# Kernel tuning notes

Hardware: AMD Instinct MI355X
Metric: run time of the kernel (lower is better)

The kernel has to match this reference:

```python
import jax, jax.numpy as jnp
import numpy as np

B, S, D = 4, 2048, 768      # batch, seq_len, embedding_dim
I = 1536                    # inner_dim = embedding_dim * up_proj_factor
H, HD = 8, 64               # num_heads, head_dim
EPS = 1e-5


def setup_inputs() -> dict:
    key = jax.random.key(0)
    ks = jax.random.split(key, 12)
    std = 0.02
    f32 = jnp.float32
    p = {}
    p["x"] = jax.random.normal(ks[0], (B, S, D), f32)
    # block LayerNorm
    p["ln_g"] = jnp.ones((D,), f32)
    p["ln_b"] = jnp.zeros((D,), f32)
    # up / down projections (bias-free, as in the module)
    p["W_up"] = jax.random.normal(ks[1], (D, I), f32) * std
    p["W_down"] = jax.random.normal(ks[2], (I, D), f32) * std
    # mLSTM cell: q/k/v projections to num_heads*head_dim
    p["Wq"] = jax.random.normal(ks[3], (I, H * HD), f32) * std
    p["Wk"] = jax.random.normal(ks[4], (I, H * HD), f32) * std
    p["Wv"] = jax.random.normal(ks[5], (I, H * HD), f32) * std
    # scalar per-head input / forget gate pre-activations
    p["Wi"] = jax.random.normal(ks[6], (I, H), f32) * std
    p["bi"] = jnp.zeros((H,), f32)
    p["Wf"] = jax.random.normal(ks[7], (I, H), f32) * std
    p["bf"] = 3.0 * jnp.ones((H,), f32)  # positive forget-gate bias init
    # output gate and cell output projection
    p["Wo"] = jax.random.normal(ks[8], (I, H * HD), f32) * std
    p["bo"] = jnp.zeros((H * HD,), f32)
    p["mh_g"] = jnp.ones((H, HD), f32)  # per-head norm scale (group norm)
    p["W_out"] = jax.random.normal(ks[9], (H * HD, I), f32) * std
    return p


def _forward(x, ln_g, ln_b, W_up, Wq, Wk, Wv, Wi, bi, Wf, bf, Wo, bo, mh_g, W_out, W_down):
    resid = x
    # LayerNorm
    mu = x.mean(-1, keepdims=True)
    var = ((x - mu) ** 2).mean(-1, keepdims=True)
    h = (x - mu) * jax.lax.rsqrt(var + EPS) * ln_g + ln_b
    # up projection
    u = h @ W_up                                    # (B,S,I)
    # mLSTM projections
    q = (u @ Wq).reshape(B, S, H, HD)
    k = (u @ Wk).reshape(B, S, H, HD) * (HD ** -0.5)
    v = (u @ Wv).reshape(B, S, H, HD)
    i_raw = u @ Wi + bi                             # (B,S,H)
    f_raw = u @ Wf + bf                             # (B,S,H)

    def step(carry, inp):
        C, n, m = carry                             # C:(B,H,HD,HD) n:(B,H,HD) m:(B,H)
        qt, kt, vt, it, ft = inp
        # log-space stabilization of exponential gates
        m_new = jnp.maximum(ft + m, it)
        ig = jnp.exp(it - m_new)
        fg = jnp.exp(ft + m - m_new)
        C = fg[..., None, None] * C + ig[..., None, None] * (vt[..., :, None] * kt[..., None, :])
        n = fg[..., None] * n + ig[..., None] * kt
        num = jnp.einsum('bhvk,bhk->bhv', C, qt)
        den = jnp.maximum(jnp.abs(jnp.einsum('bhk,bhk->bh', n, qt)), 1.0)
        return (C, n, m_new), num / den[..., None]

    xs = (jnp.moveaxis(q, 1, 0), jnp.moveaxis(k, 1, 0), jnp.moveaxis(v, 1, 0),
          jnp.moveaxis(i_raw, 1, 0), jnp.moveaxis(f_raw, 1, 0))
    C0 = jnp.zeros((B, H, HD, HD), x.dtype)
    n0 = jnp.zeros((B, H, HD), x.dtype)
    m0 = jnp.zeros((B, H), x.dtype)
    _, hts = jax.lax.scan(step, (C0, n0, m0), xs)   # (S,B,H,HD)
    ht = jnp.moveaxis(hts, 0, 1)                    # (B,S,H,HD)
    # per-head normalization (group norm, scale only)
    mu2 = ht.mean(-1, keepdims=True)
    var2 = ((ht - mu2) ** 2).mean(-1, keepdims=True)
    hn = (ht - mu2) * jax.lax.rsqrt(var2 + EPS) * mh_g
    # output gate + cell output projection
    o = jax.nn.sigmoid(u @ Wo + bo).reshape(B, S, H, HD)
    y = (o * hn).reshape(B, S, H * HD) @ W_out      # (B,S,I)
    # down projection + residual (dropout=0 -> identity)
    return resid + y @ W_down


def reference(x, ln_g, ln_b, W_up, Wq, Wk, Wv, Wi, bi, Wf, bf, Wo, bo, mh_g, W_out, W_down):
    return _forward(x, ln_g, ln_b, W_up, Wq, Wk, Wv, Wi, bi, Wf, bf, Wo, bo, mh_g, W_out, W_down)
```

## Files before the change

### kernel.cpp

```cpp
#include <hip/hip_runtime.h>
#include <hip/hip_bf16.h>
#include <stdint.h>
#include <stddef.h>

typedef __bf16 bf16_t;
typedef __bf16 bf16x4 __attribute__((ext_vector_type(4)));
typedef __bf16 bf16x8 __attribute__((ext_vector_type(8)));
typedef float  f32x4  __attribute__((ext_vector_type(4)));

#define Bsz  4
#define Ssz  2048
#define Dsz  768
#define Isz  1536
#define Hn   8
#define HDsz 64
#define NTOK (Bsz*Ssz)
#define Lc   64
#define NCH  (Ssz/Lc)
#define NBH  (Bsz*Hn)
#define NUX  1664

#define OFF_H      ((size_t)0)
#define OFF_WUPX   ((size_t)12582912)
#define OFF_WQX    ((size_t)15138816)
#define OFF_WDOWNT ((size_t)21430272)
#define OFF_WOC    ((size_t)23789568)
#define OFF_BIAS   ((size_t)24576000)
#define OFF_U      ((size_t)24580096)
#define OFF_QKVO   ((size_t)49745920)
#define OFF_KT     ((size_t)83300352)
#define OFF_VT     ((size_t)91688960)
#define OFF_IFB    ((size_t)100077568)
#define OFF_BLOC   ((size_t)100601856)
#define OFF_MHAT   ((size_t)100864000)
#define OFF_MST    ((size_t)101126144)
#define OFF_DEC    ((size_t)101130240)
#define OFF_MEND   ((size_t)101134336)
#define OFF_NG     ((size_t)101138432)
#define OFF_NST    ((size_t)101400576)
#define OFF_WOCP   ((size_t)0)
#define OFF_CSTB   ((size_t)0)
#define OFF_WOUTB  OFF_QKVO
#define OFF_G      OFF_U
#define OFF_GATED  (OFF_U + 16777216)

__device__ __forceinline__ void gload16(const void* gsrc, void* ldst) {
  __builtin_amdgcn_global_load_lds(
      (const __attribute__((address_space(1))) void*)gsrc,
      (__attribute__((address_space(3))) void*)ldst, 16, 0, 0);
}

__device__ __forceinline__ float blockReduceSum256(float v) {
  #pragma unroll
  for (int o = 1; o < 64; o <<= 1) v += __shfl_xor(v, o, 64);
  __shared__ float sh[4];
  int wid = threadIdx.x >> 6;
  __syncthreads();
  if ((threadIdx.x & 63) == 0) sh[wid] = v;
  __syncthreads();
  return sh[0] + sh[1] + sh[2] + sh[3];
}

__global__ __launch_bounds__(256) void prep_weights(
    const float* __restrict__ W_up, const float* __restrict__ Wq,
    const float* __restrict__ Wk, const float* __restrict__ Wv,
    const float* __restrict__ Wo, const float* __restrict__ W_down,
    const float* __restrict__ W_out, const float* __restrict__ bo,
    const float* __restrict__ bi, const float* __restrict__ bfv,
    bf16_t* __restrict__ wupxT, bf16_t* __restrict__ wqxT,
    bf16_t* __restrict__ wdownT, bf16_t* __restrict__ woutB,
    float* __restrict__ biasA) {
  __shared__ float tile[32][33];
  const int bid = blockIdx.x;
  const int tx = threadIdx.x, ty = threadIdx.y;
  const float* src; bf16_t* dst; int K, N, bx, by; float scale = 1.f;
  if (bid < 1152)      { int l = bid;        src = W_up;   dst = wupxT;                       K = 768;  N = 1536; bx = l % 48; by = l / 48; }
  else if (bid < 1920) { int l = bid - 1152; src = Wq;     dst = wqxT;                        K = 1536; N = 512;  bx = l % 16; by = l / 16; }
  else if (bid < 2688) { int l = bid - 1920; src = Wk;     dst = wqxT + (size_t)512 * Isz;    K = 1536; N = 512;  bx = l % 16; by = l / 16; scale = 0.125f; }
  else if (bid < 3456) { int l = bid - 2688; src = Wv;     dst = wqxT + (size_t)1024 * Isz;   K = 1536; N = 512;  bx = l % 16; by = l / 16; }
  else if (bid < 4224) { int l = bid - 3456; src = Wo;     dst = wqxT + (size_t)1536 * Isz;   K = 1536; N = 512;  bx = l % 16; by = l / 16; }
  else if (bid < 5376) { int l = bid - 4224; src = W_down; dst = wdownT;                      K = 1536; N = 768;  bx = l % 24; by = l / 24; }
  else if (bid < 6144) {
    int base = (bid - 5376) * 1024 + (ty * 32 + tx) * 4;
    #pragma unroll
    for (int e = 0; e < 4; ++e) woutB[base + e] = (bf16_t)W_out[base + e];
    return;
  } else {
    int tid = ty * 32 + tx;
    for (int i = tid; i < 528; i += 256)
      biasA[i] = (i < 512) ? bo[i] : ((i < 520) ? bi[i - 512] : bfv[i - 520]);
    return;
  }
  int n0 = bx * 32, k0 = by * 32;
  #pragma unroll
  for (int j = 0; j < 32; j += 8)
    tile[ty + j][tx] = src[(size_t)(k0 + ty + j) * N + n0 + tx];
  __syncthreads();
  #pragma unroll
  for (int j = 0; j < 32; j += 8)
    dst[(size_t)(n0 + ty + j) * K + k0 + tx] = (bf16_t)(tile[tx][ty + j] * scale);
}

__global__ __launch_bounds__(64) void build_wuif(const float* __restrict__ W_up,
                                                 const float* __restrict__ Wi,
                                                 const float* __restrict__ Wf,
                                                 bf16_t* __restrict__ dst ) {
  int d = blockIdx.x;
  int lane = threadIdx.x;
  float acc[16];
  #pragma unroll
  for (int j = 0; j < 16; ++j) acc[j] = 0.f;
  for (int i = lane; i < Isz; i += 64) {
    float w = W_up[(size_t)d * Isz + i];
    f32x4 wi0 = *(const f32x4*)&Wi[(size_t)i * 8];
    f32x4 wi1 = *(const f32x4*)&Wi[(size_t)i * 8 + 4];
    f32x4 wf0 = *(const f32x4*)&Wf[(size_t)i * 8];
    f32x4 wf1 = *(const f32x4*)&Wf[(size_t)i * 8 + 4];
    #pragma unroll
    for (int j = 0; j < 4; ++j) {
      acc[j]      += w * wi0[j];
      acc[4 + j]  += w * wi1[j];
      acc[8 + j]  += w * wf0[j];
      acc[12 + j] += w * wf1[j];
    }
  }
  #pragma unroll
  for (int j = 0; j < 16; ++j)
    #pragma unroll
    for (int o = 1; o < 64; o <<= 1) acc[j] += __shfl_xor(acc[j], o, 64);
  if (lane == 0) {
    #pragma unroll
    for (int j = 0; j < 16; ++j)
      dst[(size_t)j * Dsz + d] = (bf16_t)acc[j];
  }
}

__global__ __launch_bounds__(256) void ln_kernel(const float* __restrict__ x,
                                                 const float* __restrict__ g,
                                                 const float* __restrict__ bta,
                                                 bf16_t* __restrict__ h) {
  size_t tok = blockIdx.x;
  const float* xr = x + tok * Dsz;
  int t = threadIdx.x;
  float v[3]; float s = 0.f;
  #pragma unroll
  for (int i = 0; i < 3; ++i) { v[i] = xr[t + 256 * i]; s += v[i]; }
  s = blockReduceSum256(s);
  float mu = s * (1.f / Dsz);
  float s2 = 0.f;
  #pragma unroll
  for (int i = 0; i < 3; ++i) { float d = v[i] - mu; s2 += d * d; }
  s2 = blockReduceSum256(s2);
  float rs = rsqrtf(s2 * (1.f / Dsz) + 1e-5f);
  #pragma unroll
  for (int i = 0; i < 3; ++i) {
    int col = t + 256 * i;
    h[tok * Dsz + col] = (bf16_t)((v[i] - mu) * rs * g[col] + bta[col]);
  }
}

template<int EPI>
__global__ __launch_bounds__(512, 4) void gemm_mn(const bf16_t* __restrict__ A,
                                                  const bf16_t* __restrict__ Bt,
                                                  void* __restrict__ Cout,
                                                  const void* __restrict__ extra,
                                                  bf16_t* __restrict__ kTg,
                                                  bf16_t* __restrict__ vTg,
                                                  float* __restrict__ ifb,
                                                  int M, int N, int K) {
  __shared__ bf16_t As[256 * 64];
  __shared__ bf16_t Bs[128 * 64];
  const int t = threadIdx.x;
  const int w = t >> 6, l = t & 63;
  const int wm = w >> 1, wn = w & 1;
  const int l15 = l & 15, l4 = l >> 4;

  const int gx = gridDim.x;
  const int nwg = gx * gridDim.y;
  const int cpx = nwg >> 3;
  int bid = blockIdx.y * gx + blockIdx.x;
  int wg = (bid & 7) * cpx + (bid >> 3);
  const int tile_m = (wg / gx) * 256;
  const int tile_n = (wg % gx) * 128;

  f32x4 acc[4][4];
  #pragma unroll
  for (int m = 0; m < 4; ++m)
    #pragma unroll
    for (int n = 0; n < 4; ++n) acc[m][n] = (f32x4){0.f, 0.f, 0.f, 0.f};

  for (int k0 = 0; k0 < K; k0 += 64) {
    #pragma unroll
    for (int j = 0; j < 4; ++j) {
      int c = t + j * 512;
      int row = c >> 3;
      int ec = ((c & 7) * 8) ^ ((row & 7) << 3);
      gload16(A + (size_t)(tile_m + row) * K + k0 + ec, (char*)As + (size_t)c * 16);
    }
    #pragma unroll
    for (int j = 0; j < 2; ++j) {
      int c = t + j * 512;
      int row = c >> 3;
      int ec = ((c & 7) * 8) ^ ((row & 7) << 3);
      gload16(Bt + (size_t)(tile_n + row) * K + k0 + ec, (char*)Bs + (size_t)c * 16);
    }
    __syncthreads();
    #pragma unroll
    for (int kk = 0; kk < 2; ++kk) {
      bf16x8 aF[4], bF[4];
      #pragma unroll
      for (int m = 0; m < 4; ++m) {
        int r = wm * 64 + m * 16 + l15;
        aF[m] = *(const bf16x8*)((const char*)As + r * 128 + ((kk * 64 + l4 * 16) ^ ((r & 7) << 4)));
      }
      #pragma unroll
      for (int n = 0; n < 4; ++n) {
        int r = wn * 64 + n * 16 + l15;
        bF[n] = *(const bf16x8*)((const char*)Bs + r * 128 + ((kk * 64 + l4 * 16) ^ ((r & 7) << 4)));
      }
      #pragma unroll
      for (int m = 0; m < 4; ++m)
        #pragma unroll
        for (int n = 0; n < 4; ++n)
          acc[m][n] = __builtin_amdgcn_mfma_f32_16x16x32_bf16(aF[m], bF[n], acc[m][n], 0, 0, 0);
    }
    __syncthreads();
  }

  const int rbase = tile_m + wm * 64 + l4 * 4;
  const int cbase = tile_n + wn * 64 + l15;
  if constexpr (EPI == 5) {
    const float* bias = (const float*)extra;
    #pragma unroll
    for (int m = 0; m < 4; ++m) {
      int row0 = rbase + m * 16;
      int bb = row0 >> 11, s0 = row0 & 2047;
      #pragma unroll
      for (int n = 0; n < 4; ++n) {
        int col = cbase + n * 16;
        if (col < 512) {
          #pragma unroll
          for (int j = 0; j < 4; ++j)
            ((bf16_t*)Cout)[(size_t)(row0 + j) * 2048 + col] = (bf16_t)acc[m][n][j];
        } else if (col < 1024) {
          int hd = col - 512;
          bf16x4 pk;
          #pragma unroll
          for (int j = 0; j < 4; ++j) {
            bf16_t bv = (bf16_t)acc[m][n][j];
            ((bf16_t*)Cout)[(size_t)(row0 + j) * 2048 + col] = bv;
            pk[j] = bv;
          }
          *(bf16x4*)(kTg + ((size_t)(bb * 8 + (hd >> 6)) * 64 + (hd & 63)) * Ssz + s0) = pk;
        } else if (col < 1536) {
          int hd = col - 1024;
          bf16x4 pv;
          #pragma unroll
          for (int j = 0; j < 4; ++j) pv[j] = (bf16_t)acc[m][n][j];
          *(bf16x4*)(vTg + ((size_t)(bb * 8 + (hd >> 6)) * 64 + (hd & 63)) * Ssz + s0) = pv;
        } else {
          float b = bias[col - 1536];
          #pragma unroll
          for (int j = 0; j < 4; ++j) {
            float z = acc[m][n][j] + b;
            ((bf16_t*)Cout)[(size_t)(row0 + j) * 2048 + col] = (bf16_t)(1.f / (1.f + __expf(-z)));
          }
        }
      }
    }
  } else if constexpr (EPI == 6) {
    const float* bias = (const float*)extra;
    #pragma unroll
    for (int m = 0; m < 4; ++m)
      #pragma unroll
      for (int n = 0; n < 4; ++n) {
        int col = cbase + n * 16;
        if (col < 1536) {
          #pragma unroll
          for (int j = 0; j < 4; ++j)
            ((bf16_t*)Cout)[(size_t)(rbase + m * 16 + j) * 1536 + col] = (bf16_t)acc[m][n][j];
        } else if (col < 1552) {
          float b = bias[col - 1536];
          #pragma unroll
          for (int j = 0; j < 4; ++j)
            ifb[(size_t)(rbase + m * 16 + j) * 16 + (col - 1536)] = acc[m][n][j] + b;
        }
      }
  } else {
    #pragma unroll
    for (int m = 0; m < 4; ++m)
      #pragma unroll
      for (int n = 0; n < 4; ++n)
        #pragma unroll
        for (int j = 0; j < 4; ++j) {
          int row = rbase + m * 16 + j;
          int col = cbase + n * 16;
          float v = acc[m][n][j];
          if constexpr (EPI == 0) {
            ((bf16_t*)Cout)[(size_t)row * N + col] = (bf16_t)v;
          } else {
            ((float*)Cout)[(size_t)row * N + col] =
                v + ((const float*)extra)[(size_t)row * N + col];
          }
        }
  }
}

__global__ __launch_bounds__(256) void gemm_woc_part(const bf16_t* __restrict__ A,
                                                     const bf16_t* __restrict__ Bt,
                                                     float* __restrict__ P) {
  __shared__ bf16_t As[128 * 64];
  __shared__ bf16_t Bs[128 * 64];
  const int t = threadIdx.x;
  const int w = t >> 6, l = t & 63;
  const int tile_m = blockIdx.y * 128, tile_n = blockIdx.x * 128;
  const int kz = blockIdx.z;
  const int wr = w >> 1, wc = w & 1;
  const int lrow = l >> 3;
  const int lks = ((l & 7) * 8) ^ (lrow << 3);
  const int l15 = l & 15, l4 = l >> 4;

  f32x4 acc[4][4];
  #pragma unroll
  for (int m = 0; m < 4; ++m)
    #pragma unroll
    for (int n = 0; n < 4; ++n) acc[m][n] = (f32x4){0.f, 0.f, 0.f, 0.f};

  for (int k0 = kz * 192; k0 < kz * 192 + 192; k0 += 64) {
    #pragma unroll
    for (int i = 0; i < 4; ++i) {
      int ch = w * 4 + i;
      int row = ch * 8 + lrow;
      gload16(A  + (size_t)(tile_m + row) * Isz + k0 + lks, &As[ch * 512]);
      gload16(Bt + (size_t)(tile_n + row) * Isz + k0 + lks, &Bs[ch * 512]);
    }
    __syncthreads();
    #pragma unroll
    for (int kk = 0; kk < 2; ++kk) {
      bf16x8 af[4], bfr[4];
      #pragma unroll
      for (int m = 0; m < 4; ++m) {
        int r = wr * 64 + m * 16 + l15;
        af[m] = *(const bf16x8*)&As[r * 64 + ((kk * 32 + l4 * 8) ^ ((r & 7) << 3))];
      }
      #pragma unroll
      for (int n = 0; n < 4; ++n) {
        int r = wc * 64 + n * 16 + l15;
        bfr[n] = *(const bf16x8*)&Bs[r * 64 + ((kk * 32 + l4 * 8) ^ ((r & 7) << 3))];
      }
      #pragma unroll
      for (int m = 0; m < 4; ++m)
        #pragma unroll
        for (int n = 0; n < 4; ++n)
          acc[m][n] = __builtin_amdgcn_mfma_f32_16x16x32_bf16(af[m], bfr[n], acc[m][n], 0, 0, 0);
    }
    __syncthreads();
  }

  const int rbase = tile_m + wr * 64 + l4 * 4;
  const int cbase = tile_n + wc * 64 + l15;
  float* Pz = P + (size_t)kz * 768 * 512;
  #pragma unroll
  for (int m = 0; m < 4; ++m)
    #pragma unroll
    for (int n = 0; n < 4; ++n)
      #pragma unroll
      for (int j = 0; j < 4; ++j)
        Pz[(size_t)(rbase + m * 16 + j) * 512 + cbase + n * 16] = acc[m][n][j];
}

__global__ __launch_bounds__(256) void woc_reduce(const float* __restrict__ P,
                                                  bf16_t* __restrict__ wocT) {
  int i = blockIdx.x * 256 + threadIdx.x;
  float s = 0.f;
  #pragma unroll
  for (int z = 0; z < 8; ++z) s += P[(size_t)z * 393216 + i];
  wocT[i] = (bf16_t)s;
}

__global__ __launch_bounds__(64) void gates_a(const float* __restrict__ ifb,
                                              float* __restrict__ blocal,
                                              float* __restrict__ Mhat) {
  int bh = blockIdx.x >> 5, c = blockIdx.x & 31;
  int b = bh >> 3, h = bh & 7;
  int lane = threadIdx.x;
  size_t tok = (size_t)b * Ssz + c * Lc + lane;
  float iv = ifb[tok * 16 + h];
  float fv = ifb[tok * 16 + 8 + h];
  float bt = fv;
  #pragma unroll
  for (int d = 1; d < 64; d <<= 1) { float o = __shfl_up(bt, d, 64); if (lane >= d) bt += o; }
  float a = iv - bt;
  float pm = a;
  #pragma unroll
  for (int d = 1; d < 64; d <<= 1) { float o = __shfl_up(pm, d, 64); if (lane >= d) pm = fmaxf(pm, o); }
  blocal[(size_t)bh * Ssz + c * Lc + lane] = bt;
  Mhat[(size_t)bh * Ssz + c * Lc + lane] = bt + pm;
}

__global__ void gates_b(const float* __restrict__ blocal, const float* __restrict__ Mhat,
                        float* __restrict__ mstart, float* __restrict__ decays,
                        float* __restrict__ mend) {
  int bh = threadIdx.x;
  if (bh < NBH) {
    float M = 0.f;
    for (int c = 0; c < NCH; ++c) {
      mstart[bh * NCH + c] = M;
      float bL = blocal[(size_t)bh * Ssz + c * Lc + 63];
      float Mh = Mhat[(size_t)bh * Ssz + c * Lc + 63];
      float Mn = fmaxf(M + bL, Mh);
      decays[bh * NCH + c] = __expf(M + bL - Mn);
      mend[bh * NCH + c] = Mn;
      M = Mn;
    }
  }
}

__global__ __launch_bounds__(256) void chunk_inc_mfma(const bf16_t* __restrict__ kTg,
                                                      const bf16_t* __restrict__ vTg,
                                                      const float* __restrict__ ifb,
                                                      const float* __restrict__ blocal,
                                                      const float* __restrict__ mend,
                                                      bf16_t* __restrict__ G,
                                                      float* __restrict__ ng) {
  int bh = blockIdx.x >> 5, c = blockIdx.x & 31;
  int b = bh >> 3, h = bh & 7;
  __shared__ bf16_t Vt[64 * 64];
  __shared__ bf16_t Kw[64 * 64];
  __shared__ float wsh[64];
  const int t = threadIdx.x, w = t >> 6, l = t & 63;
  const int l15 = l & 15, l4 = l >> 4;
  if (t < 64) {
    float mL = mend[bh * NCH + c];
    float bL = blocal[(size_t)bh * Ssz + c * Lc + 63];
    float bt = blocal[(size_t)bh * Ssz + c * Lc + t];
    float iv = ifb[((size_t)b * Ssz + c * Lc + t) * 16 + h];
    wsh[t] = __expf(iv + bL - bt - mL);
  }
  __syncthreads();
  {
    const int r = l >> 3, c8 = (l & 7) * 8;
    #pragma unroll
    for (int i = 0; i < 2; ++i) {
      int seg = w * 2 + i, row = seg * 8 + r;
      gload16(vTg + ((size_t)bh * 64 + row) * Ssz + c * 64 + c8, &Vt[seg * 512]);
    }
    #pragma unroll
    for (int i = 0; i < 2; ++i) {
      int e = t + i * 256; int row = e >> 3, c0 = (e & 7) * 8;
      bf16x8 kv = *(const bf16x8*)(kTg + ((size_t)bh * 64 + row) * Ssz + c * 64 + c0);
      #pragma unroll
      for (int j = 0; j < 8; ++j) kv[j] = (bf16_t)((float)kv[j] * wsh[c0 + j]);
      *(bf16x8*)&Kw[row * 64 + c0] = kv;
    }
  }
  __syncthreads();
  f32x4 acc[4];
  #pragma unroll
  for (int n = 0; n < 4; ++n) acc[n] = (f32x4){0.f, 0.f, 0.f, 0.f};
  #pragma unroll
  for (int kk = 0; kk < 2; ++kk) {
    bf16x8 af = *(const bf16x8*)&Vt[(w * 16 + l15) * 64 + kk * 32 + l4 * 8];
    #pragma unroll
    for (int n = 0; n < 4; ++n) {
      bf16x8 bfr = *(const bf16x8*)&Kw[(n * 16 + l15) * 64 + kk * 32 + l4 * 8];
      acc[n] = __builtin_amdgcn_mfma_f32_16x16x32_bf16(af, bfr, acc[n], 0, 0, 0);
    }
  }
  size_t gb = ((size_t)bh * NCH + c) * 4096;
  #pragma unroll
  for (int n = 0; n < 4; ++n)
    #pragma unroll
    for (int j = 0; j < 4; ++j) {
      int row = w * 16 + l4 * 4 + j;
      int col = n * 16 + l15;
      G[gb + (size_t)row * 64 + col] = (bf16_t)acc[n][j];
    }
  if (t < 64) {
    float s = 0.f;
    for (int s2 = 0; s2 < 64; ++s2) s += (float)Kw[t * 64 + s2];
    ng[((size_t)bh * NCH + c) * 64 + t] = s;
  }
}

__global__ __launch_bounds__(256) void state_scan(const bf16_t* __restrict__ G,
                                                  const float* __restrict__ ng,
                                                  const float* __restrict__ decays,
                                                  bf16_t* __restrict__ CstB,
                                                  float* __restrict__ nst) {
  int gid = blockIdx.x;
  if (gid < 512) {
    int idx = gid * 256 + threadIdx.x;
    int bh = idx >> 12, e = idx & 4095;
    const float* d = decays + bh * NCH;
    float C = 0.f;
    #pragma unroll
    for (int c = 0; c < NCH; ++c) {
      size_t o = ((size_t)bh * NCH + c) * 4096 + e;
      CstB[o] = (bf16_t)C;
      C = d[c] * C + (float)G[o];
    }
  } else {
    int idx = (gid - 512) * 256 + threadIdx.x;
    int bh = idx >> 6, e = idx & 63;
    const float* d = decays + bh * NCH;
    float n = 0.f;
    #pragma unroll
    for (int c = 0; c < NCH; ++c) {
      size_t o = ((size_t)bh * NCH + c) * 64 + e;
      nst[o] = n;
      n = d[c] * n + ng[o];
    }
  }
}

__global__ __launch_bounds__(256) void intra_mfma(const bf16_t* __restrict__ qkvo,
                                                  const bf16_t* __restrict__ vTg,
                                                  const bf16_t* __restrict__ CstB,
                                                  const float* __restrict__ nst,
                                                  const float* __restrict__ ifb,
                                                  const float* __restrict__ blocal,
                                                  const float* __restrict__ Mhat,
                                                  const float* __restrict__ mstart,
                                                  const float* __restrict__ mhg,
                                                  bf16_t* __restrict__ gated) {
  int bh = blockIdx.x >> 5, c = blockIdx.x & 31;
  int b = bh >> 3, h = bh & 7;
  __shared__ bf16_t qs[64 * 64];
  __shared__ bf16_t ks[64 * 64];
  __shared__ bf16_t vTs[64 * 64];
  __shared__ bf16_t Cs[64 * 64];
  __shared__ float nin[64], den_s[64], ssrc[64], sdst[64], esc[64];
  const int t = threadIdx.x, w = t >> 6, l = t & 63;
  const int l15 = l & 15, l4 = l >> 4;
  const size_t tok0 = (size_t)b * Ssz + c * Lc;
  const size_t cbase = ((size_t)bh * NCH + c) * 4096;

  if (t < 64) {
    nin[t] = nst[((size_t)bh * NCH + c) * 64 + t];
    float bt = blocal[(size_t)bh * Ssz + c * Lc + t];
    float Mh2 = Mhat[(size_t)bh * Ssz + c * Lc + t];
    float Mc = mstart[bh * NCH + c];
    float iv = ifb[(tok0 + t) * 16 + h];
    float mt = fmaxf(Mc + bt, Mh2);
    ssrc[t] = iv - bt;
    sdst[t] = bt - mt;
    esc[t]  = __expf(Mc + bt - mt);
  }
  {
    const int r = l >> 3, c8 = (l & 7) * 8;
    #pragma unroll
    for (int i = 0; i < 2; ++i) {
      int seg = w * 2 + i, row = seg * 8 + r;
      gload16(qkvo + (tok0 + row) * 2048 + h * 64 + c8,          &qs[seg * 512]);
      gload16(qkvo + (tok0 + row) * 2048 + 512 + h * 64 + c8,    &ks[seg * 512]);
      gload16(vTg + ((size_t)bh * 64 + row) * Ssz + c * 64 + c8, &vTs[seg * 512]);
      gload16(CstB + cbase + seg * 512 + l * 8,                  &Cs[seg * 512]);
    }
  }
  __syncthreads();

  f32x4 aS[4];
  #pragma unroll
  for (int n = 0; n < 4; ++n) aS[n] = (f32x4){0.f, 0.f, 0.f, 0.f};
  #pragma unroll
  for (int kk = 0; kk < 2; ++kk) {
    bf16x8 af = *(const bf16x8*)&qs[(w * 16 + l15) * 64 + kk * 32 + l4 * 8];
    #pragma unroll
    for (int n = 0; n < 4; ++n) {
      bf16x8 bfr = *(const bf16x8*)&ks[(n * 16 + l15) * 64 + kk * 32 + l4 * 8];
      aS[n] = __builtin_amdgcn_mfma_f32_16x16x32_bf16(af, bfr, aS[n], 0, 0, 0);
    }
  }
  {
    int row = w * 16 + (l >> 2);
    int c0 = (l & 3) * 16;
    float e = esc[row];
    #pragma unroll
    for (int i2 = 0; i2 < 2; ++i2) {
      bf16x8 v8 = *(const bf16x8*)&qs[row * 64 + c0 + i2 * 8];
      #pragma unroll
      for (int j = 0; j < 8; ++j) v8[j] = (bf16_t)((float)v8[j] * e);
      *(bf16x8*)&qs[row * 64 + c0 + i2 * 8] = v8;
    }
  }
  float rs[4] = {0.f, 0.f, 0.f, 0.f};
  #pragma unroll
  for (int n = 0; n < 4; ++n) {
    int col = n * 16 + l15;
    float es = ssrc[col];
    #pragma unroll
    for (int j = 0; j < 4; ++j) {
      int row = w * 16 + l4 * 4 + j;
      float p = (col <= row) ? aS[n][j] * __expf(es + sdst[row]) : 0.f;
      aS[n][j] = p;
      rs[j] += p;
    }
  }
  #pragma unroll
  for (int j = 0; j < 4; ++j) {
    rs[j] += __shfl_xor(rs[j], 1, 64);
    rs[j] += __shfl_xor(rs[j], 2, 64);
    rs[j] += __shfl_xor(rs[j], 4, 64);
    rs[j] += __shfl_xor(rs[j], 8, 64);
  }
  if (l15 == 0) {
    #pragma unroll
    for (int j = 0; j < 4; ++j) den_s[w * 16 + l4 * 4 + j] = rs[j];
  }
  __syncthreads();

  #pragma unroll
  for (int n = 0; n < 4; ++n)
    #pragma unroll
    for (int j = 0; j < 4; ++j)
      ks[(w * 16 + l4 * 4 + j) * 64 + n * 16 + l15] = (bf16_t)aS[n][j];

  {
    int row = w * 16 + (l >> 2);
    int c0 = (l & 3) * 16;
    float part = 0.f;
    #pragma unroll
    for (int i2 = 0; i2 < 16; ++i2)
      part += (float)qs[row * 64 + c0 + i2] * nin[c0 + i2];
    part += __shfl_xor(part, 1, 64);
    part += __shfl_xor(part, 2, 64);
    if ((l & 3) == 0)
      den_s[row] = fmaxf(fabsf(den_s[row] + part), 1.0f);
  }
  __syncthreads();

  f32x4 aO[4];
  #pragma unroll
  for (int n = 0; n < 4; ++n) aO[n] = (f32x4){0.f, 0.f, 0.f, 0.f};
  #pragma unroll
  for (int kk = 0; kk < 2; ++kk) {
    bf16x8 afP = *(const bf16x8*)&ks[(w * 16 + l15) * 64 + kk * 32 + l4 * 8];
    bf16x8 afQ = *(const bf16x8*)&qs[(w * 16 + l15) * 64 + kk * 32 + l4 * 8];
    #pragma unroll
    for (int n = 0; n < 4; ++n) {
      bf16x8 bV = *(const bf16x8*)&vTs[(n * 16 + l15) * 64 + kk * 32 + l4 * 8];
      bf16x8 bC = *(const bf16x8*)&Cs[(n * 16 + l15) * 64 + kk * 32 + l4 * 8];
      aO[n] = __builtin_amdgcn_mfma_f32_16x16x32_bf16(afP, bV, aO[n], 0, 0, 0);
      aO[n] = __builtin_amdgcn_mfma_f32_16x16x32_bf16(afQ, bC, aO[n], 0, 0, 0);
    }
  }

  #pragma unroll
  for (int j = 0; j < 4; ++j) {
    int row = w * 16 + l4 * 4 + j;
    float rinv = 1.f / den_s[row];
    float ov[4];
    #pragma unroll
    for (int n = 0; n < 4; ++n) ov[n] = aO[n][j] * rinv;
    float s = ov[0] + ov[1] + ov[2] + ov[3];
    s += __shfl_xor(s, 1, 64); s += __shfl_xor(s, 2, 64);
    s += __shfl_xor(s, 4, 64); s += __shfl_xor(s, 8, 64);
    float mu = s * (1.f / 64.f);
    float s2 = 0.f;
    #pragma unroll
    for (int n = 0; n < 4; ++n) { float d = ov[n] - mu; s2 += d * d; }
    s2 += __shfl_xor(s2, 1, 64); s2 += __shfl_xor(s2, 2, 64);
    s2 += __shfl_xor(s2, 4, 64); s2 += __shfl_xor(s2, 8, 64);
    float rstd = rsqrtf(s2 * (1.f / 64.f) + 1e-5f);
    size_t tok = tok0 + row;
    #pragma unroll
    for (int n = 0; n < 4; ++n) {
      int colh = n * 16 + l15;
      float og = (float)qkvo[tok * 2048 + 1536 + h * 64 + colh];
      float hn = (ov[n] - mu) * rstd * mhg[h * 64 + colh];
      gated[tok * 512 + h * 64 + colh] = (bf16_t)(og * hn);
    }
  }
}

extern "C" void kernel_launch(void* const* d_in, const int* in_sizes, int n_in,
                              void* d_out, int out_size, void* d_ws, size_t ws_size,
                              hipStream_t stream) {
  const float* x     = (const float*)d_in[0];
  const float* ln_g  = (const float*)d_in[1];
  const float* ln_b  = (const float*)d_in[2];
  const float* W_up  = (const float*)d_in[3];
  const float* W_down= (const float*)d_in[4];
  const float* Wq    = (const float*)d_in[5];
  const float* Wk    = (const float*)d_in[6];
  const float* Wv    = (const float*)d_in[7];
  const float* Wi    = (const float*)d_in[8];
  const float* bi    = (const float*)d_in[9];
  const float* Wf    = (const float*)d_in[10];
  const float* bfv   = (const float*)d_in[11];
  const float* Wo    = (const float*)d_in[12];
  const float* bo    = (const float*)d_in[13];
  const float* mh_g  = (const float*)d_in[14];
  const float* W_out = (const float*)d_in[15];

  char* ws = (char*)d_ws;
  bf16_t* hbuf   = (bf16_t*)(ws + OFF_H);
  bf16_t* wupxT  = (bf16_t*)(ws + OFF_WUPX);
  bf16_t* wqxT   = (bf16_t*)(ws + OFF_WQX);
  bf16_t* wdownT = (bf16_t*)(ws + OFF_WDOWNT);
  bf16_t* wocT   = (bf16_t*)(ws + OFF_WOC);
  float*  biasA  = (float*)(ws + OFF_BIAS);
  bf16_t* ubuf   = (bf16_t*)(ws + OFF_U);
  bf16_t* qkvob  = (bf16_t*)(ws + OFF_QKVO);
  bf16_t* woutB  = (bf16_t*)(ws + OFF_WOUTB);
  float*  wocP   = (float*)(ws + OFF_WOCP);
  bf16_t* kTg    = (bf16_t*)(ws + OFF_KT);
  bf16_t* vTg    = (bf16_t*)(ws + OFF_VT);
  float*  ifb    = (float*)(ws + OFF_IFB);
  float*  bloc   = (float*)(ws + OFF_BLOC);
  float*  Mh     = (float*)(ws + OFF_MHAT);
  float*  mst    = (float*)(ws + OFF_MST);
  float*  decays = (float*)(ws + OFF_DEC);
  float*  mendb  = (float*)(ws + OFF_MEND);
  float*  ngbuf  = (float*)(ws + OFF_NG);
  float*  nst    = (float*)(ws + OFF_NST);
  bf16_t* CstB   = (bf16_t*)(ws + OFF_CSTB);
  bf16_t* Gbuf   = (bf16_t*)(ws + OFF_G);
  bf16_t* gbuf   = (bf16_t*)(ws + OFF_GATED);

  prep_weights<<<6145, dim3(32, 8), 0, stream>>>(W_up, Wq, Wk, Wv, Wo, W_down, W_out,
                                                 bo, bi, bfv, wupxT, wqxT, wdownT, woutB, biasA);
  build_wuif<<<Dsz, 64, 0, stream>>>(W_up, Wi, Wf, wupxT + (size_t)1536 * Dsz);
  gemm_woc_part<<<dim3(4, 6, 8), 256, 0, stream>>>(wdownT, woutB, wocP);
  woc_reduce<<<1536, 256, 0, stream>>>(wocP, wocT);

  ln_kernel<<<NTOK, 256, 0, stream>>>(x, ln_g, ln_b, hbuf);

  gemm_mn<6><<<dim3(NUX / 128, NTOK / 256), 512, 0, stream>>>(hbuf, wupxT, ubuf, biasA + 512, nullptr, nullptr, ifb, NTOK, NUX, Dsz);
  gemm_mn<5><<<dim3(2048 / 128, NTOK / 256), 512, 0, stream>>>(ubuf, wqxT, qkvob, biasA, kTg, vTg, nullptr, NTOK, 2048, Isz);

  gates_a<<<NBH * NCH, 64, 0, stream>>>(ifb, bloc, Mh);
  gates_b<<<1, 32, 0, stream>>>(bloc, Mh, mst, decays, mendb);
  chunk_inc_mfma<<<NBH * NCH, 256, 0, stream>>>(kTg, vTg, ifb, bloc, mendb, Gbuf, ngbuf);
  state_scan<<<520, 256, 0, stream>>>(Gbuf, ngbuf, decays, CstB, nst);
  intra_mfma<<<NBH * NCH, 256, 0, stream>>>(qkvob, vTg, CstB, nst, ifb, bloc, Mh, mst, mh_g, gbuf);

  gemm_mn<3><<<dim3(Dsz / 128, NTOK / 256), 512, 0, stream>>>(gbuf, wocT, (float*)d_out, x, nullptr, nullptr, nullptr, NTOK, Dsz, 512);
}
```

Before: 175.1 us.

## Fold W_up into q/k/v/o weights and compute gates with a small MFMA kernel

Precomputes the product of the q/k/v/o weight stack with W_up (via a split-K weight GEMM plus reduction), so the activation path goes straight from the LayerNorm output to q/k/v/o with K=768. This removes the separate up-projection GEMM and the materialised u buffer. The input and forget gate pre-activations move into a dedicated thin MFMA kernel over h. The cost is extra per-call weight-prep GEMM work and different bf16 rounding, since the product is rounded once instead of u being rounded.

```diff
diff --git a/kernel.cpp b/kernel.cpp
--- a/kernel.cpp
+++ b/kernel.cpp
@@ -18,31 +18,32 @@
 #define Lc   64
 #define NCH  (Ssz/Lc)
 #define NBH  (Bsz*Hn)
-#define NUX  1664
 
 #define OFF_H      ((size_t)0)
-#define OFF_WUPX   ((size_t)12582912)
-#define OFF_WQX    ((size_t)15138816)
-#define OFF_WDOWNT ((size_t)21430272)
-#define OFF_WOC    ((size_t)23789568)
-#define OFF_BIAS   ((size_t)24576000)
-#define OFF_U      ((size_t)24580096)
-#define OFF_QKVO   ((size_t)49745920)
-#define OFF_KT     ((size_t)83300352)
-#define OFF_VT     ((size_t)91688960)
-#define OFF_IFB    ((size_t)100077568)
-#define OFF_BLOC   ((size_t)100601856)
-#define OFF_MHAT   ((size_t)100864000)
-#define OFF_MST    ((size_t)101126144)
-#define OFF_DEC    ((size_t)101130240)
-#define OFF_MEND   ((size_t)101134336)
-#define OFF_NG     ((size_t)101138432)
-#define OFF_NST    ((size_t)101400576)
-#define OFF_WOCP   ((size_t)0)
-#define OFF_CSTB   ((size_t)0)
-#define OFF_WOUTB  OFF_QKVO
-#define OFF_G      OFF_U
-#define OFF_GATED  (OFF_U + 16777216)
+#define OFF_WQX    ((size_t)12582912)
+#define OFF_WQC    ((size_t)18874368)
+#define OFF_WDOWNT ((size_t)22020096)
+#define OFF_WOC    ((size_t)24379392)
+#define OFF_WUPB   ((size_t)25165824)
+#define OFF_WUIF   ((size_t)27525120)
+#define OFF_BIAS   ((size_t)27549696)
+#define OFF_WOUTB  ((size_t)27553792)
+#define OFF_QKVO   ((size_t)29126656)
+#define OFF_KT     ((size_t)62681088)
+#define OFF_VT     ((size_t)71069696)
+#define OFF_GATED  ((size_t)79458304)
+#define OFF_G      ((size_t)87846912)
+#define OFF_IFB    ((size_t)96235520)
+#define OFF_BLOC   ((size_t)96759808)
+#define OFF_MHAT   ((size_t)97021952)
+#define OFF_MST    ((size_t)97284096)
+#define OFF_DEC    ((size_t)97288192)
+#define OFF_MEND   ((size_t)97292288)
+#define OFF_NG     ((size_t)97296384)
+#define OFF_NST    ((size_t)97558528)
+#define OFF_WOCP   OFF_H
+#define OFF_CSTB   OFF_H
+#define OFF_COMPP  OFF_QKVO
 
 __device__ __forceinline__ void gload16(const void* gsrc, void* ldst) {
   __builtin_amdgcn_global_load_lds(
@@ -67,23 +68,27 @@
     const float* __restrict__ Wo, const float* __restrict__ W_down,
     const float* __restrict__ W_out, const float* __restrict__ bo,
     const float* __restrict__ bi, const float* __restrict__ bfv,
-    bf16_t* __restrict__ wupxT, bf16_t* __restrict__ wqxT,
-    bf16_t* __restrict__ wdownT, bf16_t* __restrict__ woutB,
+    bf16_t* __restrict__ wqxT, bf16_t* __restrict__ wdownT,
+    bf16_t* __restrict__ woutB, bf16_t* __restrict__ wupB,
     float* __restrict__ biasA) {
   __shared__ float tile[32][33];
   const int bid = blockIdx.x;
   const int tx = threadIdx.x, ty = threadIdx.y;
   const float* src; bf16_t* dst; int K, N, bx, by; float scale = 1.f;
-  if (bid < 1152)      { int l = bid;        src = W_up;   dst = wupxT;                       K = 768;  N = 1536; bx = l % 48; by = l / 48; }
-  else if (bid < 1920) { int l = bid - 1152; src = Wq;     dst = wqxT;                        K = 1536; N = 512;  bx = l % 16; by = l / 16; }
-  else if (bid < 2688) { int l = bid - 1920; src = Wk;     dst = wqxT + (size_t)512 * Isz;    K = 1536; N = 512;  bx = l % 16; by = l / 16; scale = 0.125f; }
-  else if (bid < 3456) { int l = bid - 2688; src = Wv;     dst = wqxT + (size_t)1024 * Isz;   K = 1536; N = 512;  bx = l % 16; by = l / 16; }
-  else if (bid < 4224) { int l = bid - 3456; src = Wo;     dst = wqxT + (size_t)1536 * Isz;   K = 1536; N = 512;  bx = l % 16; by = l / 16; }
-  else if (bid < 5376) { int l = bid - 4224; src = W_down; dst = wdownT;                      K = 1536; N = 768;  bx = l % 24; by = l / 24; }
-  else if (bid < 6144) {
-    int base = (bid - 5376) * 1024 + (ty * 32 + tx) * 4;
+  if (bid < 768)       { int l = bid;        src = Wq;     dst = wqxT;                      K = 1536; N = 512; bx = l % 16; by = l / 16; }
+  else if (bid < 1536) { int l = bid - 768;  src = Wk;     dst = wqxT + (size_t)512 * Isz;  K = 1536; N = 512; bx = l % 16; by = l / 16; scale = 0.125f; }
+  else if (bid < 2304) { int l = bid - 1536; src = Wv;     dst = wqxT + (size_t)1024 * Isz; K = 1536; N = 512; bx = l % 16; by = l / 16; }
+  else if (bid < 3072) { int l = bid - 2304; src = Wo;     dst = wqxT + (size_t)1536 * Isz; K = 1536; N = 512; bx = l % 16; by = l / 16; }
+  else if (bid < 4224) { int l = bid - 3072; src = W_down; dst = wdownT;                    K = 1536; N = 768; bx = l % 24; by = l / 24; }
+  else if (bid < 4992) {
+    int base = (bid - 4224) * 1024 + (ty * 32 + tx) * 4;
     #pragma unroll
     for (int e = 0; e < 4; ++e) woutB[base + e] = (bf16_t)W_out[base + e];
+    return;
+  } else if (bid < 6144) {
+    int base = (bid - 4992) * 1024 + (ty * 32 + tx) * 4;
+    #pragma unroll
+    for (int e = 0; e < 4; ++e) wupB[base + e] = (bf16_t)W_up[base + e];
     return;
   } else {
     int tid = ty * 32 + tx;
@@ -132,6 +137,81 @@
     #pragma unroll
     for (int j = 0; j < 16; ++j)
       dst[(size_t)j * Dsz + d] = (bf16_t)acc[j];
+  }
+}
+
+__global__ __launch_bounds__(256) void gemm_partk(const bf16_t* __restrict__ A,
+                                                  const bf16_t* __restrict__ Bt,
+                                                  float* __restrict__ P,
+                                                  int M, int N, int Ktot, int kslice) {
+  __shared__ bf16_t As[128 * 64];
+  __shared__ bf16_t Bs[128 * 64];
+  const int t = threadIdx.x;
+  const int w = t >> 6, l = t & 63;
+  const int tile_m = blockIdx.y * 128, tile_n = blockIdx.x * 128;
+  const int kz = blockIdx.z;
+  const int wr = w >> 1, wc = w & 1;
+  const int lrow = l >> 3;
+  const int lks = ((l & 7) * 8) ^ (lrow << 3);
+  const int l15 = l & 15, l4 = l >> 4;
+
+  f32x4 acc[4][4];
+  #pragma unroll
+  for (int m = 0; m < 4; ++m)
+    #pragma unroll
+    for (int n = 0; n < 4; ++n) acc[m][n] = (f32x4){0.f, 0.f, 0.f, 0.f};
+
+  for (int k0 = kz * kslice; k0 < kz * kslice + kslice; k0 += 64) {
+    #pragma unroll
+    for (int i = 0; i < 4; ++i) {
+      int ch = w * 4 + i;
+      int row = ch * 8 + lrow;
+      gload16(A  + (size_t)(tile_m + row) * Ktot + k0 + lks, &As[ch * 512]);
+      gload16(Bt + (size_t)(tile_n + row) * Ktot + k0 + lks, &Bs[ch * 512]);
+    }
+    __syncthreads();
+    #pragma unroll
+    for (int kk = 0; kk < 2; ++kk) {
+      bf16x8 af[4], bfr[4];
+      #pragma unroll
+      for (int m = 0; m < 4; ++m) {
+        int r = wr * 64 + m * 16 + l15;
+        af[m] = *(const bf16x8*)&As[r * 64 + ((kk * 32 + l4 * 8) ^ ((r & 7) << 3))];
+      }
+      #pragma unroll
+      for (int n = 0; n < 4; ++n) {
+        int r = wc * 64 + n * 16 + l15;
+        bfr[n] = *(const bf16x8*)&Bs[r * 64 + ((kk * 32 + l4 * 8) ^ ((r & 7) << 3))];
+      }
+      #pragma unroll
+      for (int m = 0; m < 4; ++m)
+        #pragma unroll
+        for (int n = 0; n < 4; ++n)
+          acc[m][n] = __builtin_amdgcn_mfma_f32_16x16x32_bf16(af[m], bfr[n], acc[m][n], 0, 0, 0);
+    }
+    __syncthreads();
+  }
+
+  const int rbase = tile_m + wr * 64 + l4 * 4;
+  const int cbase = tile_n + wc * 64 + l15;
+  float* Pz = P + (size_t)kz * M * N;
+  #pragma unroll
+  for (int m = 0; m < 4; ++m)
+    #pragma unroll
+    for (int n = 0; n < 4; ++n)
+      #pragma unroll
+      for (int j = 0; j < 4; ++j)
+        Pz[(size_t)(rbase + m * 16 + j) * N + cbase + n * 16] = acc[m][n][j];
+}
+
+__global__ __launch_bounds__(256) void partk_reduce(const float* __restrict__ P,
+                                                    bf16_t* __restrict__ out,
+                                                    int nelem, int nz) {
+  int i = blockIdx.x * 256 + threadIdx.x;
+  if (i < nelem) {
+    float s = 0.f;
+    for (int z = 0; z < nz; ++z) s += P[(size_t)z * nelem + i];
+    out[i] = (bf16_t)s;
   }
 }
 
@@ -159,6 +239,54 @@
   }
 }
 
+__global__ __launch_bounds__(256) void ifproj_mfma(const bf16_t* __restrict__ h,
+                                                   const bf16_t* __restrict__ wuifT,
+                                                   const float* __restrict__ bi,
+                                                   const float* __restrict__ bfv,
+                                                   float* __restrict__ ifb) {
+  __shared__ bf16_t As[128 * 64];
+  __shared__ bf16_t Bs[16 * 64];
+  const int t = threadIdx.x, w = t >> 6, l = t & 63;
+  const int l15 = l & 15, l4 = l >> 4;
+  const int lrow = l >> 3, lk = (l & 7) * 8;
+  const int tile_m = blockIdx.x * 128;
+  f32x4 acc[2];
+  acc[0] = (f32x4){0.f, 0.f, 0.f, 0.f};
+  acc[1] = (f32x4){0.f, 0.f, 0.f, 0.f};
+
+  for (int k0 = 0; k0 < Dsz; k0 += 64) {
+    #pragma unroll
+    for (int i = 0; i < 4; ++i) {
+      int ch = w * 4 + i;
+      int row = ch * 8 + lrow;
+      gload16(h + (size_t)(tile_m + row) * Dsz + k0 + lk, &As[ch * 512]);
+    }
+    if (t < 128) {
+      int rr = t >> 3, c0 = (t & 7) * 8;
+      *(bf16x8*)&Bs[rr * 64 + c0] = *(const bf16x8*)(wuifT + (size_t)rr * Dsz + k0 + c0);
+    }
+    __syncthreads();
+    #pragma unroll
+    for (int kk = 0; kk < 2; ++kk) {
+      bf16x8 bfr = *(const bf16x8*)&Bs[l15 * 64 + kk * 32 + l4 * 8];
+      #pragma unroll
+      for (int m = 0; m < 2; ++m) {
+        bf16x8 af = *(const bf16x8*)&As[(w * 32 + m * 16 + l15) * 64 + kk * 32 + l4 * 8];
+        acc[m] = __builtin_amdgcn_mfma_f32_16x16x32_bf16(af, bfr, acc[m], 0, 0, 0);
+      }
+    }
+    __syncthreads();
+  }
+  float bias = (l15 < 8) ? bi[l15] : bfv[l15 - 8];
+  #pragma unroll
+  for (int m = 0; m < 2; ++m)
+    #pragma unroll
+    for (int j = 0; j < 4; ++j) {
+      int row = tile_m + w * 32 + m * 16 + l4 * 4 + j;
+      ifb[(size_t)row * 16 + l15] = acc[m][j] + bias;
+    }
+}
+
 template<int EPI>
 __global__ __launch_bounds__(512, 4) void gemm_mn(const bf16_t* __restrict__ A,
                                                   const bf16_t* __restrict__ Bt,
@@ -166,7 +294,6 @@
                                                   const void* __restrict__ extra,
                                                   bf16_t* __restrict__ kTg,
                                                   bf16_t* __restrict__ vTg,
-                                                  float* __restrict__ ifb,
                                                   int M, int N, int K) {
   __shared__ bf16_t As[256 * 64];
   __shared__ bf16_t Bs[128 * 64];
@@ -268,24 +395,6 @@
         }
       }
     }
-  } else if constexpr (EPI == 6) {
-    const float* bias = (const float*)extra;
-    #pragma unroll
-    for (int m = 0; m < 4; ++m)
-      #pragma unroll
-      for (int n = 0; n < 4; ++n) {
-        int col = cbase + n * 16;
-        if (col < 1536) {
-          #pragma unroll
-          for (int j = 0; j < 4; ++j)
-            ((bf16_t*)Cout)[(size_t)(rbase + m * 16 + j) * 1536 + col] = (bf16_t)acc[m][n][j];
-        } else if (col < 1552) {
-          float b = bias[col - 1536];
-          #pragma unroll
-          for (int j = 0; j < 4; ++j)
-            ifb[(size_t)(rbase + m * 16 + j) * 16 + (col - 1536)] = acc[m][n][j] + b;
-        }
-      }
   } else {
     #pragma unroll
     for (int m = 0; m < 4; ++m)
@@ -295,87 +404,10 @@
         for (int j = 0; j < 4; ++j) {
           int row = rbase + m * 16 + j;
           int col = cbase + n * 16;
-          float v = acc[m][n][j];
-          if constexpr (EPI == 0) {
-            ((bf16_t*)Cout)[(size_t)row * N + col] = (bf16_t)v;
-          } else {
-            ((float*)Cout)[(size_t)row * N + col] =
-                v + ((const float*)extra)[(size_t)row * N + col];
-          }
+          ((float*)Cout)[(size_t)row * N + col] =
+              acc[m][n][j] + ((const float*)extra)[(size_t)row * N + col];
         }
   }
-}
-
-__global__ __launch_bounds__(256) void gemm_woc_part(const bf16_t* __restrict__ A,
-                                                     const bf16_t* __restrict__ Bt,
-                                                     float* __restrict__ P) {
-  __shared__ bf16_t As[128 * 64];
-  __shared__ bf16_t Bs[128 * 64];
-  const int t = threadIdx.x;
-  const int w = t >> 6, l = t & 63;
-  const int tile_m = blockIdx.y * 128, tile_n = blockIdx.x * 128;
-  const int kz = blockIdx.z;
-  const int wr = w >> 1, wc = w & 1;
-  const int lrow = l >> 3;
-  const int lks = ((l & 7) * 8) ^ (lrow << 3);
-  const int l15 = l & 15, l4 = l >> 4;
-
-  f32x4 acc[4][4];
-  #pragma unroll
-  for (int m = 0; m < 4; ++m)
-    #pragma unroll
-    for (int n = 0; n < 4; ++n) acc[m][n] = (f32x4){0.f, 0.f, 0.f, 0.f};
-
-  for (int k0 = kz * 192; k0 < kz * 192 + 192; k0 += 64) {
-    #pragma unroll
-    for (int i = 0; i < 4; ++i) {
-      int ch = w * 4 + i;
-      int row = ch * 8 + lrow;
-      gload16(A  + (size_t)(tile_m + row) * Isz + k0 + lks, &As[ch * 512]);
-      gload16(Bt + (size_t)(tile_n + row) * Isz + k0 + lks, &Bs[ch * 512]);
-    }
-    __syncthreads();
-    #pragma unroll
-    for (int kk = 0; kk < 2; ++kk) {
-      bf16x8 af[4], bfr[4];
-      #pragma unroll
-      for (int m = 0; m < 4; ++m) {
-        int r = wr * 64 + m * 16 + l15;
-        af[m] = *(const bf16x8*)&As[r * 64 + ((kk * 32 + l4 * 8) ^ ((r & 7) << 3))];
-      }
-      #pragma unroll
-      for (int n = 0; n < 4; ++n) {
-        int r = wc * 64 + n * 16 + l15;
-        bfr[n] = *(const bf16x8*)&Bs[r * 64 + ((kk * 32 + l4 * 8) ^ ((r & 7) << 3))];
-      }
-      #pragma unroll
-      for (int m = 0; m < 4; ++m)
-        #pragma unroll
-        for (int n = 0; n < 4; ++n)
-          acc[m][n] = __builtin_amdgcn_mfma_f32_16x16x32_bf16(af[m], bfr[n], acc[m][n], 0, 0, 0);
-    }
-    __syncthreads();
-  }
-
-  const int rbase = tile_m + wr * 64 + l4 * 4;
-  const int cbase = tile_n + wc * 64 + l15;
-  float* Pz = P + (size_t)kz * 768 * 512;
-  #pragma unroll
-  for (int m = 0; m < 4; ++m)
-    #pragma unroll
-    for (int n = 0; n < 4; ++n)
-      #pragma unroll
-      for (int j = 0; j < 4; ++j)
-        Pz[(size_t)(rbase + m * 16 + j) * 512 + cbase + n * 16] = acc[m][n][j];
-}
-
-__global__ __launch_bounds__(256) void woc_reduce(const float* __restrict__ P,
-                                                  bf16_t* __restrict__ wocT) {
-  int i = blockIdx.x * 256 + threadIdx.x;
-  float s = 0.f;
-  #pragma unroll
-  for (int z = 0; z < 8; ++z) s += P[(size_t)z * 393216 + i];
-  wocT[i] = (bf16_t)s;
 }
 
 __global__ __launch_bounds__(64) void gates_a(const float* __restrict__ ifb,
@@ -696,17 +728,19 @@
 
   char* ws = (char*)d_ws;
   bf16_t* hbuf   = (bf16_t*)(ws + OFF_H);
-  bf16_t* wupxT  = (bf16_t*)(ws + OFF_WUPX);
   bf16_t* wqxT   = (bf16_t*)(ws + OFF_WQX);
+  bf16_t* wqcT   = (bf16_t*)(ws + OFF_WQC);
   bf16_t* wdownT = (bf16_t*)(ws + OFF_WDOWNT);
   bf16_t* wocT   = (bf16_t*)(ws + OFF_WOC);
+  bf16_t* wupB   = (bf16_t*)(ws + OFF_WUPB);
+  bf16_t* wuifT  = (bf16_t*)(ws + OFF_WUIF);
   float*  biasA  = (float*)(ws + OFF_BIAS);
-  bf16_t* ubuf   = (bf16_t*)(ws + OFF_U);
+  bf16_t* woutB  = (bf16_t*)(ws + OFF_WOUTB);
   bf16_t* qkvob  = (bf16_t*)(ws + OFF_QKVO);
-  bf16_t* woutB  = (bf16_t*)(ws + OFF_WOUTB);
-  float*  wocP   = (float*)(ws + OFF_WOCP);
   bf16_t* kTg    = (bf16_t*)(ws + OFF_KT);
   bf16_t* vTg    = (bf16_t*)(ws + OFF_VT);
+  bf16_t* gbuf   = (bf16_t*)(ws + OFF_GATED);
+  bf16_t* Gbuf   = (bf16_t*)(ws + OFF_G);
   float*  ifb    = (float*)(ws + OFF_IFB);
   float*  bloc   = (float*)(ws + OFF_BLOC);
   float*  Mh     = (float*)(ws + OFF_MHAT);
@@ -715,20 +749,23 @@
   float*  mendb  = (float*)(ws + OFF_MEND);
   float*  ngbuf  = (float*)(ws + OFF_NG);
   float*  nst    = (float*)(ws + OFF_NST);
+  float*  wocP   = (float*)(ws + OFF_WOCP);
+  float*  compP  = (float*)(ws + OFF_COMPP);
   bf16_t* CstB   = (bf16_t*)(ws + OFF_CSTB);
-  bf16_t* Gbuf   = (bf16_t*)(ws + OFF_G);
-  bf16_t* gbuf   = (bf16_t*)(ws + OFF_GATED);
 
   prep_weights<<<6145, dim3(32, 8), 0, stream>>>(W_up, Wq, Wk, Wv, Wo, W_down, W_out,
-                                                 bo, bi, bfv, wupxT, wqxT, wdownT, woutB, biasA);
-  build_wuif<<<Dsz, 64, 0, stream>>>(W_up, Wi, Wf, wupxT + (size_t)1536 * Dsz);
-  gemm_woc_part<<<dim3(4, 6, 8), 256, 0, stream>>>(wdownT, woutB, wocP);
-  woc_reduce<<<1536, 256, 0, stream>>>(wocP, wocT);
+                                                 bo, bi, bfv, wqxT, wdownT, woutB, wupB, biasA);
+  build_wuif<<<Dsz, 64, 0, stream>>>(W_up, Wi, Wf, wuifT);
+
+  gemm_partk<<<dim3(6, 16, 4), 256, 0, stream>>>(wqxT, wupB, compP, 2048, 768, 1536, 384);
+  partk_reduce<<<6144, 256, 0, stream>>>(compP, wqcT, 2048 * 768, 4);
+  gemm_partk<<<dim3(4, 6, 8), 256, 0, stream>>>(wdownT, woutB, wocP, 768, 512, 1536, 192);
+  partk_reduce<<<1536, 256, 0, stream>>>(wocP, wocT, 768 * 512, 8);
 
   ln_kernel<<<NTOK, 256, 0, stream>>>(x, ln_g, ln_b, hbuf);
-
-  gemm_mn<6><<<dim3(NUX / 128, NTOK / 256), 512, 0, stream>>>(hbuf, wupxT, ubuf, biasA + 512, nullptr, nullptr, ifb, NTOK, NUX, Dsz);
-  gemm_mn<5><<<dim3(2048 / 128, NTOK / 256), 512, 0, stream>>>(ubuf, wqxT, qkvob, biasA, kTg, vTg, nullptr, NTOK, 2048, Isz);
+  ifproj_mfma<<<NTOK / 128, 256, 0, stream>>>(hbuf, wuifT, bi, bfv, ifb);
+
+  gemm_mn<5><<<dim3(2048 / 128, NTOK / 256), 512, 0, stream>>>(hbuf, wqcT, qkvob, biasA, kTg, vTg, NTOK, 2048, Dsz);
 
   gates_a<<<NBH * NCH, 64, 0, stream>>>(ifb, bloc, Mh);
   gates_b<<<1, 32, 0, stream>>>(bloc, Mh, mst, decays, mendb);
@@ -736,5 +773,5 @@
   state_scan<<<520, 256, 0, stream>>>(Gbuf, ngbuf, decays, CstB, nst);
   intra_mfma<<<NBH * NCH, 256, 0, stream>>>(qkvob, vTg, CstB, nst, ifb, bloc, Mh, mst, mh_g, gbuf);
 
-  gemm_mn<3><<<dim3(Dsz / 128, NTOK / 256), 512, 0, stream>>>(gbuf, wocT, (float*)d_out, x, nullptr, nullptr, nullptr, NTOK, Dsz, 512);
-}
+  gemm_mn<3><<<dim3(Dsz / 128, NTOK / 256), 512, 0, stream>>>(gbuf, wocT, (float*)d_out, x, nullptr, nullptr, NTOK, Dsz, 512);
+}
```

After: 163.2 us. -6.8%, faster.
